# Kernel optimization log

Measured on AMD Instinct MI355X. Metric: run time of the kernel, lower is better.

## Reference

```python
import jax, jax.numpy as jnp
import numpy as np

B, D, E, G, P, H = 8192, 2048, 8, 4, 512, 192
T, DT, TAU, VTH, VRESET = 20, 0.001, 0.02, 0.5, 0.0
DELTA0, KTOP, KROUTE, PREDW = 7.0, 32, 2, 0.1


def setup_inputs() -> dict:
    key = jax.random.key(0)
    ks = jax.random.split(key, 12)
    s = 0.02
    return {
        "query_embedding": jax.random.normal(ks[0], (B, D), jnp.float32),
        "Wg": jax.random.normal(ks[1], (2, E), jnp.float32) * s,
        "bg": jnp.zeros((E,), jnp.float32),
        "Wp": jax.random.normal(ks[2], (2, E), jnp.float32) * s,
        "bp": jnp.zeros((E,), jnp.float32),
        "Wgg": jax.random.normal(ks[3], (2, G), jnp.float32) * s,
        "bgg": jnp.zeros((G,), jnp.float32),
        "W1": jax.random.normal(ks[4], (E, D, P), jnp.float32) * (1.0 / np.sqrt(D)),
        "b1": jnp.zeros((E, P), jnp.float32),
        "W2": jax.random.normal(ks[5], (E, P, D), jnp.float32) * (1.0 / np.sqrt(P)),
        "b2": jnp.zeros((E, D), jnp.float32),
    }


def reference(query_embedding, Wg, bg, Wp, bp, Wgg, bgg, W1, b1, W2, b2):
    x = query_embedding  # [B, D], already embed_dim -> no pad/slice
    dtype = x.dtype

    # --- Phasor bank temporal features on per-row mean ---
    qm = jnp.mean(x, axis=-1)  # [B]
    freqs = DELTA0 * jnp.arange(1, H + 1, dtype=dtype)  # [H]
    ang = qm[:, None] * freqs[None, :]  # [B, H]
    temporal = jnp.concatenate([jnp.cos(ang), jnp.sin(ang)], axis=-1)  # [B, 2H]

    # --- Spiking attention over top-K |x| indices (LIF over T steps) ---
    topk_idx = jax.lax.top_k(jnp.abs(x), KTOP)[1]  # [B, K]
    rows = jnp.arange(B)[:, None]
    I = jnp.zeros((B, D), dtype).at[rows, topk_idx].add(1.0)  # input current [B, vocab=D]

    def lif_step(v, _):
        v = v * (1.0 - DT / TAU) + I
        spike = (v >= VTH).astype(dtype)
        v = jnp.where(spike > 0, VRESET, v)
        return v, spike

    _, spikes = jax.lax.scan(lif_step, jnp.zeros((B, D), dtype), None, length=T)
    attention_gains = jnp.mean(spikes, axis=0)  # [B, D] spike rates

    # --- Bio gating inputs ---
    gate_in = jnp.stack([jnp.mean(temporal, axis=-1), jnp.mean(attention_gains, axis=-1)], axis=-1)  # [B, 2]

    gate_logits = gate_in @ Wg + bg  # [B, E]
    gate_logits = gate_logits - PREDW * (gate_in @ Wp + bp)

    # group routing bias: experts grouped round-robin i % G
    group_logits = gate_in @ Wgg + bgg  # [B, G]
    gmap = jax.nn.one_hot(jnp.arange(E) % G, G, dtype=dtype)  # [E, G]
    gate_logits = gate_logits + group_logits @ gmap.T

    gate_weights = jax.nn.softmax(gate_logits, axis=-1)  # temperature = 1

    # top-k routing + renormalization
    _, tidx = jax.lax.top_k(gate_weights, KROUTE)
    mask = jnp.zeros_like(gate_weights).at[rows, tidx].set(1.0)
    gated = gate_weights * mask
    gate_weights = gated / (jnp.sum(gated, axis=-1, keepdims=True) + 1e-9)

    # --- Dense MLP experts (bottleneck P = hidden // 4) ---
    h = jax.nn.relu(jnp.einsum('bd,edp->ebp', x, W1) + b1[:, None, :])  # [E, B, P]
    expert_out = jnp.einsum('ebp,eph->ebh', h, W2) + b2[:, None, :]  # [E, B, D]

    # gate-weighted combine
    context = jnp.einsum('be,ebh->bh', gate_weights, expert_out)  # [B, D]
    return context
```

## Files before the change

### kernel.cpp

```cpp
#include <hip/hip_runtime.h>
#include <stdint.h>

#define NB 8192
#define ND 2048
#define NE 8
#define NG 4
#define NP 512
#define NH 192

typedef _Float16 half_t;
typedef half_t f16x8 __attribute__((ext_vector_type(8)));
typedef float f32x4 __attribute__((ext_vector_type(4)));

__device__ __forceinline__ void gload16(const void* g, void* l) {
  __builtin_amdgcn_global_load_lds(
      (const __attribute__((address_space(1))) void*)g,
      (__attribute__((address_space(3))) void*)l, 16, 0, 0);
}

__global__ __launch_bounds__(256) void k_pre(
    const float* __restrict__ x, half_t* __restrict__ xh,
    const float* __restrict__ W1, const float* __restrict__ W2,
    half_t* __restrict__ w1t, half_t* __restrict__ w2t,
    const float* __restrict__ Wg, const float* __restrict__ bg,
    const float* __restrict__ Wp, const float* __restrict__ bp,
    const float* __restrict__ Wgg, const float* __restrict__ bgg,
    int* __restrict__ e0a, int* __restrict__ e1a,
    float* __restrict__ w0a, float* __restrict__ w1a)
{
  const int t = threadIdx.x;

  if (blockIdx.x >= NB) {
    int id = blockIdx.x - NB;
    const int which = id >> 12;
    id &= 4095;
    const int R = which ? NP : ND;
    const int C = which ? ND : NP;
    const float* src = which ? W2 : W1;
    half_t* dst = which ? w2t : w1t;
    const int tiles_c = C >> 5;
    const int tiles_per_e = (R >> 6) * tiles_c;
    int e = id / tiles_per_e;
    int rem = id - e * tiles_per_e;
    int tr = rem / tiles_c, tc = rem - tr * tiles_c;
    __shared__ float tile[64][33];
    const int lc = t & 31, lr = t >> 5;
    const float* s = src + (size_t)e * R * C + (size_t)(tr * 64) * C + tc * 32;
#pragma unroll
    for (int i = 0; i < 8; i++)
      tile[lr + i * 8][lc] = s[(size_t)(lr + i * 8) * C + lc];
    __syncthreads();
    const int n = t >> 3, kc = (t & 7) * 8;
    __align__(16) half_t hb[8];
#pragma unroll
    for (int j = 0; j < 8; j++) hb[j] = (half_t)tile[kc + j][n];
    half_t* d = dst + (size_t)e * R * C + (size_t)(tc * 32 + n) * R + tr * 64 + kc;
    *reinterpret_cast<int4*>(d) = *reinterpret_cast<const int4*>(hb);
    return;
  }

  const int b = blockIdx.x;
  const float* xr = x + (size_t)b * ND;
  const float4 v0 = ((const float4*)xr)[t * 2];
  const float4 v1 = ((const float4*)xr)[t * 2 + 1];
  float f[8] = {v0.x, v0.y, v0.z, v0.w, v1.x, v1.y, v1.z, v1.w};
  double s = 0.0;
  __align__(16) half_t hb[8];
#pragma unroll
  for (int i = 0; i < 8; i++) { s += (double)f[i]; hb[i] = (half_t)f[i]; }
  *reinterpret_cast<int4*>(xh + (size_t)b * ND + t * 8) = *reinterpret_cast<const int4*>(hb);

#pragma unroll
  for (int m = 32; m >= 1; m >>= 1) s += __shfl_xor(s, m);
  __shared__ double part[4];
  __shared__ double qm_s;
  if ((t & 63) == 0) part[t >> 6] = s;
  __syncthreads();
  if (t == 0) qm_s = (part[0] + part[1] + part[2] + part[3]) / (double)ND;
  __syncthreads();

  const double q = qm_s;
  double g = 0.0;
  if (t < 192) {
    double ang = q * (7.0 * (double)(t + 1));
    g = cos(ang) + sin(ang);
  }
#pragma unroll
  for (int m = 32; m >= 1; m >>= 1) g += __shfl_xor(g, m);
  __shared__ double gp[4];
  if ((t & 63) == 0) gp[t >> 6] = g;
  __syncthreads();

  if (t < 64) {
    const double tm = (gp[0] + gp[1] + gp[2] + gp[3]) / (2.0 * (double)NH);
    const double gi1 = 32.0 / 2048.0;
    double lg = -1.0e300;
    if (t < 8) {
      const int e = t, gg = e & 3;
      lg = tm * (double)Wg[e] + gi1 * (double)Wg[NE + e] + (double)bg[e];
      lg -= 0.1 * (tm * (double)Wp[e] + gi1 * (double)Wp[NE + e] + (double)bp[e]);
      lg += tm * (double)Wgg[gg] + gi1 * (double)Wgg[NG + gg] + (double)bgg[gg];
    }
    double mx = lg;
#pragma unroll
    for (int m = 4; m >= 1; m >>= 1) mx = fmax(mx, __shfl_xor(mx, m));
    double pe = 0.0;
    if (t < 8) pe = exp(lg - mx);
    double ps = pe;
#pragma unroll
    for (int m = 4; m >= 1; m >>= 1) ps += __shfl_xor(ps, m);

    double lgs[8], pes[8];
#pragma unroll
    for (int e = 0; e < 8; e++) { lgs[e] = __shfl(lg, e); pes[e] = __shfl(pe, e); }

    if (t == 0) {
      int e0 = 0;
      for (int e = 1; e < NE; e++) if (lgs[e] > lgs[e0]) e0 = e;
      int e1 = (e0 == 0) ? 1 : 0;
      for (int e = 0; e < NE; e++) if (e != e0 && lgs[e] > lgs[e1]) e1 = e;
      const double p0 = pes[e0] / ps;
      const double p1 = pes[e1] / ps;
      const double den = p0 + p1 + 1e-9;
      e0a[b] = e0; e1a[b] = e1;
      w0a[b] = (float)(p0 / den);
      w1a[b] = (float)(p1 / den);
    }
  }
}

__global__ __launch_bounds__(256) void k_bucket(
    const int* __restrict__ e0a, const int* __restrict__ e1a,
    const float* __restrict__ w0a, const float* __restrict__ w1a,
    int* __restrict__ rowl, float* __restrict__ wl, int* __restrict__ cnt,
    int* __restrict__ pos0a, int* __restrict__ pos1a,
    int* __restrict__ rowlp, int* __restrict__ cntp,
    int* __restrict__ ticket, int* __restrict__ pbase,
    int* __restrict__ i16b, int* __restrict__ i16m, int* __restrict__ n16,
    int* __restrict__ ipp, int* __restrict__ ipm, int* __restrict__ np)
{
  const int t = threadIdx.x;
  const int r = blockIdx.x * 256 + t;
  __shared__ int hist[16], base[16], cursor[16];
  __shared__ int histp[64], basep[64], cursorp[64];
  __shared__ int lastf;
  if (t < 16) { hist[t] = 0; cursor[t] = 0; }
  if (t < 64) { histp[t] = 0; cursorp[t] = 0; }
  __syncthreads();

  const int e0 = e0a[r], e1 = e1a[r];
  const int p = e0 * 8 + e1;
  atomicAdd(&hist[e0], 1);
  atomicAdd(&hist[8 + e1], 1);
  atomicAdd(&histp[p], 1);
  __syncthreads();
  if (t < 16) base[t] = atomicAdd(&cnt[t], hist[t]);
  if (t < 64) basep[t] = atomicAdd(&cntp[t], histp[t]);
  __syncthreads();

  int p0 = atomicAdd(&cursor[e0], 1);
  int idx0 = base[e0] + p0;
  rowl[e0 * NB + idx0] = r;
  wl[e0 * NB + idx0] = w0a[r];
  pos0a[r] = idx0;

  int p1 = atomicAdd(&cursor[8 + e1], 1);
  int idx1 = base[8 + e1] + p1;
  rowl[(8 + e1) * NB + idx1] = r;
  wl[(8 + e1) * NB + idx1] = w1a[r];
  pos1a[r] = idx1;

  int pp = atomicAdd(&cursorp[p], 1);
  rowlp[p * NB + basep[p] + pp] = r;

  __threadfence();
  __syncthreads();
  if (t == 0) lastf = (atomicAdd(ticket, 1) == (int)gridDim.x - 1);
  __syncthreads();
  if (lastf) {
    if (t == 0) {
      int c[16];
#pragma unroll
      for (int i = 0; i < 16; i++) c[i] = atomicAdd(&cnt[i], 0);
      int s = 0;
#pragma unroll
      for (int i = 0; i < 16; i++) { pbase[i] = s; s += c[i]; }
      int k = 0;
      for (int bb = 0; bb < 16; bb++)
        for (int m0 = 0; m0 < c[bb]; m0 += 128) { i16b[k] = bb; i16m[k] = m0; k++; }
      *n16 = k;
    } else if (t == 64) {
      int c[64];
#pragma unroll
      for (int i = 0; i < 64; i++) c[i] = atomicAdd(&cntp[i], 0);
      int k = 0;
      for (int pq = 0; pq < 64; pq++)
        for (int m0 = 0; m0 < c[pq]; m0 += 128) { ipp[k] = pq; ipm[k] = m0; k++; }
      *np = k;
    }
  }
}

__global__ __launch_bounds__(256, 2) void k_gemm1(
    const half_t* __restrict__ xh, const half_t* __restrict__ w1t,
    const float* __restrict__ b1,
    const int* __restrict__ rowl, const float* __restrict__ wl,
    const int* __restrict__ cnt, const int* __restrict__ pbase,
    const int* __restrict__ i16b, const int* __restrict__ i16m,
    const int* __restrict__ n16, half_t* __restrict__ Hbuf)
{
  const int wi = blockIdx.y;
  if (wi >= *n16) return;
  const int bucket = i16b[wi];
  const int m0 = i16m[wi];
  const int count = cnt[bucket];
  const int e = bucket & 7;
  const int n0 = blockIdx.x * 256;
  const int t = threadIdx.x;

  __shared__ __align__(16) half_t As[3][128 * 32];
  __shared__ __align__(16) half_t Bs[3][256 * 32];
  __shared__ int rows_s[128];
  __shared__ float ws_s[128];

  if (t < 128) {
    int mi = m0 + t;
    int idx = bucket * NB + (mi < count ? mi : m0);
    rows_s[t] = rowl[idx];
    ws_s[t] = wl[idx];
  }
  __syncthreads();

  const int w = t >> 6, lane = t & 63;
  const int cA0 = (w * 2) * 64 + lane, cA1 = cA0 + 64;
  const int rA0 = cA0 >> 2, rA1 = cA1 >> 2;
  const int kA0 = ((cA0 & 3) ^ ((rA0 >> 1) & 3)) * 8;
  const int kA1 = ((cA1 & 3) ^ ((rA1 >> 1) & 3)) * 8;
  const half_t* gA0 = xh + (size_t)rows_s[rA0] * ND + kA0;
  const half_t* gA1 = xh + (size_t)rows_s[rA1] * ND + kA1;
  const half_t* w1te = w1t + (size_t)e * NP * ND;
  const int cB0 = (w * 4) * 64 + lane, cB1 = cB0 + 64, cB2 = cB0 + 128, cB3 = cB0 + 192;
  const int rB0 = cB0 >> 2, rB1 = cB1 >> 2, rB2 = cB2 >> 2, rB3 = cB3 >> 2;
  const half_t* gB0 = w1te + (size_t)(n0 + rB0) * ND + ((cB0 & 3) ^ ((rB0 >> 1) & 3)) * 8;
  const half_t* gB1 = w1te + (size_t)(n0 + rB1) * ND + ((cB1 & 3) ^ ((rB1 >> 1) & 3)) * 8;
  const half_t* gB2 = w1te + (size_t)(n0 + rB2) * ND + ((cB2 & 3) ^ ((rB2 >> 1) & 3)) * 8;
  const half_t* gB3 = w1te + (size_t)(n0 + rB3) * ND + ((cB3 & 3) ^ ((rB3 >> 1) & 3)) * 8;

  const int wr = w >> 1, wc = w & 1;
  const int lrow = lane & 15, lk = lane >> 4;
  const int lko = (lk ^ ((lrow >> 1) & 3)) * 8;

  f32x4 acc[4][8];
#pragma unroll
  for (int i = 0; i < 4; i++)
#pragma unroll
    for (int j = 0; j < 8; j++) {
      acc[i][j][0] = 0.f; acc[i][j][1] = 0.f; acc[i][j][2] = 0.f; acc[i][j][3] = 0.f;
    }

  auto stage = [&](int bi, int tt) {
    const int kk = tt * 32;
    half_t* la = &As[bi][w * 1024];
    gload16(gA0 + kk, la);
    gload16(gA1 + kk, la + 512);
    half_t* lb = &Bs[bi][w * 2048];
    gload16(gB0 + kk, lb);
    gload16(gB1 + kk, lb + 512);
    gload16(gB2 + kk, lb + 1024);
    gload16(gB3 + kk, lb + 1536);
  };
  auto compute = [&](int bi) {
    f16x8 af[4], bf[8];
#pragma unroll
    for (int i = 0; i < 4; i++)
      af[i] = *reinterpret_cast<const f16x8*>(&As[bi][(wr * 64 + i * 16 + lrow) * 32 + lko]);
#pragma unroll
    for (int n = 0; n < 8; n++)
      bf[n] = *reinterpret_cast<const f16x8*>(&Bs[bi][(wc * 128 + n * 16 + lrow) * 32 + lko]);
#pragma unroll
    for (int mi = 0; mi < 4; mi++)
#pragma unroll
      for (int ni = 0; ni < 8; ni++)
        acc[mi][ni] = __builtin_amdgcn_mfma_f32_16x16x32_f16(af[mi], bf[ni], acc[mi][ni], 0, 0, 0);
  };

  stage(0, 0);
  stage(1, 1);
  asm volatile("s_waitcnt vmcnt(6)" ::: "memory");
  __builtin_amdgcn_s_barrier();
  for (int t3 = 0; t3 < 60; t3 += 3) {
    stage(2, t3 + 2); compute(0);
    asm volatile("s_waitcnt vmcnt(6) lgkmcnt(0)" ::: "memory");
    __builtin_amdgcn_s_barrier();
    stage(0, t3 + 3); compute(1);
    asm volatile("s_waitcnt vmcnt(6) lgkmcnt(0)" ::: "memory");
    __builtin_amdgcn_s_barrier();
    stage(1, t3 + 4); compute(2);
    asm volatile("s_waitcnt vmcnt(6) lgkmcnt(0)" ::: "memory");
    __builtin_amdgcn_s_barrier();
  }
  stage(2, 62); compute(0);
  asm volatile("s_waitcnt vmcnt(6) lgkmcnt(0)" ::: "memory");
  __builtin_amdgcn_s_barrier();
  stage(0, 63); compute(1);
  asm volatile("s_waitcnt vmcnt(6) lgkmcnt(0)" ::: "memory");
  __builtin_amdgcn_s_barrier();
  compute(2);
  asm volatile("s_waitcnt vmcnt(0) lgkmcnt(0)" ::: "memory");
  __builtin_amdgcn_s_barrier();
  compute(0);

  const int pb = pbase[bucket];
#pragma unroll
  for (int mi = 0; mi < 4; mi++) {
#pragma unroll
    for (int i = 0; i < 4; i++) {
      int lm = wr * 64 + mi * 16 + lk * 4 + i;
      if (m0 + lm < count) {
        size_t prow = (size_t)(pb + m0 + lm) * NP;
        float wcoef = ws_s[lm];
#pragma unroll
        for (int ni = 0; ni < 8; ni++) {
          int col = n0 + wc * 128 + ni * 16 + lrow;
          float v = acc[mi][ni][i] + b1[e * NP + col];
          v = v > 0.f ? v : 0.f;
          Hbuf[prow + col] = (half_t)(v * wcoef);
        }
      }
    }
  }
}

__global__ __launch_bounds__(256) void k_gemm2p(
    const half_t* __restrict__ Hbuf, const half_t* __restrict__ w2t,
    const float* __restrict__ b2,
    const int* __restrict__ rowlp, const int* __restrict__ cntp,
    const int* __restrict__ pbase,
    const int* __restrict__ pos0a, const int* __restrict__ pos1a,
    const float* __restrict__ w0a, const float* __restrict__ w1a,
    const int* __restrict__ ipp, const int* __restrict__ ipm,
    const int* __restrict__ np, float* __restrict__ out)
{
  const int wi = blockIdx.y;
  if (wi >= *np) return;
  const int p = ipp[wi];
  const int m0 = ipm[wi];
  const int count = cntp[p];
  const int e0 = p >> 3, e1 = p & 7;
  const int n0 = blockIdx.x * 128;
  const int t = threadIdx.x;

  __shared__ __align__(16) half_t As[3][128 * 32];
  __shared__ __align__(16) half_t Bs[3][128 * 32];
  __shared__ int h0_s[128], h1_s[128], rs_s[128];
  __shared__ float w0_s[128], w1_s[128];

  if (t < 128) {
    int mi = m0 + t;
    int r = rowlp[p * NB + (mi < count ? mi : m0)];
    rs_s[t] = r;
    h0_s[t] = pbase[e0] + pos0a[r];
    h1_s[t] = pbase[8 + e1] + pos1a[r];
    w0_s[t] = w0a[r];
    w1_s[t] = w1a[r];
  }
  __syncthreads();

  const int w = t >> 6, lane = t & 63;
  const int c0 = w * 128 + lane, c1 = c0 + 64;
  const int row0 = c0 >> 2, ch0 = c0 & 3;
  const int row1 = c1 >> 2, ch1 = c1 & 3;
  const int sw0 = (row0 >> 1) & 3, sw1 = (row1 >> 1) & 3;
  const half_t* w2e0 = w2t + (size_t)e0 * ND * NP;
  const half_t* w2e1 = w2t + (size_t)e1 * ND * NP;
  const half_t* sa00 = Hbuf + (size_t)h0_s[row0] * NP + ((ch0 ^ sw0) * 8);
  const half_t* sa01 = Hbuf + (size_t)h0_s[row1] * NP + ((ch1 ^ sw1) * 8);
  const half_t* sa10 = Hbuf + (size_t)h1_s[row0] * NP + ((ch0 ^ sw0) * 8);
  const half_t* sa11 = Hbuf + (size_t)h1_s[row1] * NP + ((ch1 ^ sw1) * 8);
  const half_t* pB00 = w2e0 + (size_t)(n0 + row0) * NP + ((ch0 ^ sw0) * 8);
  const half_t* pB01 = w2e0 + (size_t)(n0 + row1) * NP + ((ch1 ^ sw1) * 8);
  const half_t* pB10 = w2e1 + (size_t)(n0 + row0) * NP + ((ch0 ^ sw0) * 8);
  const half_t* pB11 = w2e1 + (size_t)(n0 + row1) * NP + ((ch1 ^ sw1) * 8);

  const int wr = w >> 1, wc = w & 1;
  const int lrow = lane & 15, lk = lane >> 4;
  const int lko = (lk ^ ((lrow >> 1) & 3)) * 8;

  f32x4 acc[4][4];
#pragma unroll
  for (int i = 0; i < 4; i++)
#pragma unroll
    for (int j = 0; j < 4; j++) {
      acc[i][j][0] = 0.f; acc[i][j][1] = 0.f; acc[i][j][2] = 0.f; acc[i][j][3] = 0.f;
    }

  const int NT = 32;

  auto stage = [&](int bi, int tt) {
    const int kk = (tt & 15) * 32;
    half_t* la = &As[bi][w * 1024];
    half_t* lb = &Bs[bi][w * 1024];
    if (tt & 16) {
      gload16(sa10 + kk, la);
      gload16(sa11 + kk, la + 512);
      gload16(pB10 + kk, lb);
      gload16(pB11 + kk, lb + 512);
    } else {
      gload16(sa00 + kk, la);
      gload16(sa01 + kk, la + 512);
      gload16(pB00 + kk, lb);
      gload16(pB01 + kk, lb + 512);
    }
  };
  auto compute = [&](int bi) {
    f16x8 af[4], bf[4];
#pragma unroll
    for (int i = 0; i < 4; i++) {
      af[i] = *reinterpret_cast<const f16x8*>(&As[bi][(wr * 64 + i * 16 + lrow) * 32 + lko]);
      bf[i] = *reinterpret_cast<const f16x8*>(&Bs[bi][(wc * 64 + i * 16 + lrow) * 32 + lko]);
    }
#pragma unroll
    for (int mi = 0; mi < 4; mi++)
#pragma unroll
      for (int ni = 0; ni < 4; ni++)
        acc[mi][ni] = __builtin_amdgcn_mfma_f32_16x16x32_f16(af[mi], bf[ni], acc[mi][ni], 0, 0, 0);
  };

  stage(0, 0);
  stage(1, 1);
  asm volatile("s_waitcnt vmcnt(4)" ::: "memory");
  __builtin_amdgcn_s_barrier();
#pragma unroll
  for (int tt = 0; tt < NT; ++tt) {
    if (tt + 2 < NT) stage((tt + 2) % 3, tt + 2);
    compute(tt % 3);
    if (tt + 1 < NT) {
      if (tt + 2 < NT) asm volatile("s_waitcnt vmcnt(4) lgkmcnt(0)" ::: "memory");
      else             asm volatile("s_waitcnt vmcnt(0) lgkmcnt(0)" ::: "memory");
      __builtin_amdgcn_s_barrier();
    }
  }

  float b20[4], b21[4];
#pragma unroll
  for (int ni = 0; ni < 4; ni++) {
    int col = n0 + wc * 64 + ni * 16 + lrow;
    b20[ni] = b2[e0 * ND + col];
    b21[ni] = b2[e1 * ND + col];
  }
#pragma unroll
  for (int mi = 0; mi < 4; mi++) {
#pragma unroll
    for (int i = 0; i < 4; i++) {
      int lm = wr * 64 + mi * 16 + lk * 4 + i;
      if (m0 + lm < count) {
        int r = rs_s[lm];
        float wb0 = w0_s[lm], wb1 = w1_s[lm];
        float* orow = out + (size_t)r * ND;
#pragma unroll
        for (int ni = 0; ni < 4; ni++) {
          int col = n0 + wc * 64 + ni * 16 + lrow;
          orow[col] = acc[mi][ni][i] + wb0 * b20[ni] + wb1 * b21[ni];
        }
      }
    }
  }
}

extern "C" void kernel_launch(void* const* d_in, const int* in_sizes, int n_in,
                              void* d_out, int out_size, void* d_ws, size_t ws_size,
                              hipStream_t stream)
{
  const float* x   = (const float*)d_in[0];
  const float* Wg  = (const float*)d_in[1];
  const float* bg  = (const float*)d_in[2];
  const float* Wp  = (const float*)d_in[3];
  const float* bp  = (const float*)d_in[4];
  const float* Wgg = (const float*)d_in[5];
  const float* bgg = (const float*)d_in[6];
  const float* W1  = (const float*)d_in[7];
  const float* b1  = (const float*)d_in[8];
  const float* W2  = (const float*)d_in[9];
  const float* b2  = (const float*)d_in[10];
  float* out = (float*)d_out;

  char* ws = (char*)d_ws;
  size_t off = 0;
  const size_t OFF_XH   = off; off += (size_t)NB * ND * 2;
  const size_t OFF_W1T  = off; off += (size_t)NE * NP * ND * 2;
  const size_t OFF_W2T  = off; off += (size_t)NE * ND * NP * 2;
  const size_t OFF_H    = off; off += (size_t)(2 * NB + 128) * NP * 2;
  const size_t OFF_ROWL = off; off += (size_t)16 * NB * 4;
  const size_t OFF_WL   = off; off += (size_t)16 * NB * 4;
  const size_t OFF_ROWLP= off; off += (size_t)64 * NB * 4;
  const size_t OFF_CNT  = off; off += 64;
  const size_t OFF_CNTP = off; off += 256;
  const size_t OFF_TKT  = off; off += 64;
  const size_t OFF_PB   = off; off += 64;
  const size_t OFF_E0   = off; off += (size_t)NB * 4;
  const size_t OFF_E1   = off; off += (size_t)NB * 4;
  const size_t OFF_W0   = off; off += (size_t)NB * 4;
  const size_t OFF_W1A  = off; off += (size_t)NB * 4;
  const size_t OFF_POS0 = off; off += (size_t)NB * 4;
  const size_t OFF_POS1 = off; off += (size_t)NB * 4;
  const size_t OFF_I16B = off; off += 1024;
  const size_t OFF_I16M = off; off += 1024;
  const size_t OFF_N16  = off; off += 64;
  const size_t OFF_IPP  = off; off += 1024;
  const size_t OFF_IPM  = off; off += 1024;
  const size_t OFF_NP   = off; off += 64;

  half_t* xh   = (half_t*)(ws + OFF_XH);
  half_t* w1t  = (half_t*)(ws + OFF_W1T);
  half_t* w2t  = (half_t*)(ws + OFF_W2T);
  half_t* Hbuf = (half_t*)(ws + OFF_H);
  int*    rowl = (int*)(ws + OFF_ROWL);
  float*  wl   = (float*)(ws + OFF_WL);
  int*    rowlp= (int*)(ws + OFF_ROWLP);
  int*    cnt  = (int*)(ws + OFF_CNT);
  int*    cntp = (int*)(ws + OFF_CNTP);
  int*    tkt  = (int*)(ws + OFF_TKT);
  int*    pb   = (int*)(ws + OFF_PB);
  int*    e0a  = (int*)(ws + OFF_E0);
  int*    e1a  = (int*)(ws + OFF_E1);
  float*  w0a  = (float*)(ws + OFF_W0);
  float*  w1a  = (float*)(ws + OFF_W1A);
  int*    pos0a= (int*)(ws + OFF_POS0);
  int*    pos1a= (int*)(ws + OFF_POS1);
  int*    i16b = (int*)(ws + OFF_I16B);
  int*    i16m = (int*)(ws + OFF_I16M);
  int*    n16  = (int*)(ws + OFF_N16);
  int*    ipp  = (int*)(ws + OFF_IPP);
  int*    ipm  = (int*)(ws + OFF_IPM);
  int*    np   = (int*)(ws + OFF_NP);

  hipMemsetAsync(cnt, 0, 64 + 256 + 64, stream);
  k_pre<<<NB + 8192, 256, 0, stream>>>(x, xh, W1, W2, w1t, w2t,
                                       Wg, bg, Wp, bp, Wgg, bgg,
                                       e0a, e1a, w0a, w1a);
  k_bucket<<<NB / 256, 256, 0, stream>>>(e0a, e1a, w0a, w1a, rowl, wl, cnt,
                                         pos0a, pos1a, rowlp, cntp,
                                         tkt, pb, i16b, i16m, n16, ipp, ipm, np);
  k_gemm1<<<dim3(2, 144, 1), 256, 0, stream>>>(xh, w1t, b1, rowl, wl, cnt, pb,
                                               i16b, i16m, n16, Hbuf);
  k_gemm2p<<<dim3(16, 128, 1), 256, 0, stream>>>(Hbuf, w2t, b2, rowlp, cntp, pb,
                                                 pos0a, pos1a, w0a, w1a, ipp, ipm, np, out);
}
```

Before: 333.1 us.

## Use 8-wave 512-thread blocks for both expert GEMMs, widen gemm2 N tile

k_gemm1 keeps its 128x256 block tile but splits it across 8 waves of 64x64 each instead of 4 waves of 64x128, which halves per-wave accumulators and global-to-LDS loads. k_gemm2p doubles its N tile to 256 so more A-tile reuse happens per block, also with 8 waves, and its grid in x is halved. Wait counts are adjusted to the new per-thread load counts. The launch_bounds(512,4) hint asks for high occupancy, which can force tight register budgets and spills. The large LDS footprint may also prevent that occupancy from being reached.

Measured after the change: 327.5 us. No clear change (-1.7%).

```diff
diff --git a/kernel.cpp b/kernel.cpp
--- a/kernel.cpp
+++ b/kernel.cpp
@@ -201,7 +201,7 @@
   }
 }
 
-__global__ __launch_bounds__(256, 2) void k_gemm1(
+__global__ __launch_bounds__(512, 4) void k_gemm1(
     const half_t* __restrict__ xh, const half_t* __restrict__ w1t,
     const float* __restrict__ b1,
     const int* __restrict__ rowl, const float* __restrict__ wl,
@@ -232,78 +232,69 @@
   __syncthreads();
 
   const int w = t >> 6, lane = t & 63;
-  const int cA0 = (w * 2) * 64 + lane, cA1 = cA0 + 64;
-  const int rA0 = cA0 >> 2, rA1 = cA1 >> 2;
-  const int kA0 = ((cA0 & 3) ^ ((rA0 >> 1) & 3)) * 8;
-  const int kA1 = ((cA1 & 3) ^ ((rA1 >> 1) & 3)) * 8;
-  const half_t* gA0 = xh + (size_t)rows_s[rA0] * ND + kA0;
-  const half_t* gA1 = xh + (size_t)rows_s[rA1] * ND + kA1;
+  const int rA = w * 16 + (lane >> 2);
+  const int kA = ((lane & 3) ^ ((rA >> 1) & 3)) * 8;
+  const half_t* gA = xh + (size_t)rows_s[rA] * ND + kA;
   const half_t* w1te = w1t + (size_t)e * NP * ND;
-  const int cB0 = (w * 4) * 64 + lane, cB1 = cB0 + 64, cB2 = cB0 + 128, cB3 = cB0 + 192;
-  const int rB0 = cB0 >> 2, rB1 = cB1 >> 2, rB2 = cB2 >> 2, rB3 = cB3 >> 2;
-  const half_t* gB0 = w1te + (size_t)(n0 + rB0) * ND + ((cB0 & 3) ^ ((rB0 >> 1) & 3)) * 8;
-  const half_t* gB1 = w1te + (size_t)(n0 + rB1) * ND + ((cB1 & 3) ^ ((rB1 >> 1) & 3)) * 8;
-  const half_t* gB2 = w1te + (size_t)(n0 + rB2) * ND + ((cB2 & 3) ^ ((rB2 >> 1) & 3)) * 8;
-  const half_t* gB3 = w1te + (size_t)(n0 + rB3) * ND + ((cB3 & 3) ^ ((rB3 >> 1) & 3)) * 8;
-
-  const int wr = w >> 1, wc = w & 1;
+  const int rB0 = w * 32 + (lane >> 2), rB1 = rB0 + 16;
+  const int kB0 = ((lane & 3) ^ ((rB0 >> 1) & 3)) * 8;
+  const int kB1 = ((lane & 3) ^ ((rB1 >> 1) & 3)) * 8;
+  const half_t* gB0 = w1te + (size_t)(n0 + rB0) * ND + kB0;
+  const half_t* gB1 = w1te + (size_t)(n0 + rB1) * ND + kB1;
+
+  const int wr = w >> 2, wn = w & 3;
   const int lrow = lane & 15, lk = lane >> 4;
   const int lko = (lk ^ ((lrow >> 1) & 3)) * 8;
 
-  f32x4 acc[4][8];
+  f32x4 acc[4][4];
 #pragma unroll
   for (int i = 0; i < 4; i++)
 #pragma unroll
-    for (int j = 0; j < 8; j++) {
+    for (int j = 0; j < 4; j++) {
       acc[i][j][0] = 0.f; acc[i][j][1] = 0.f; acc[i][j][2] = 0.f; acc[i][j][3] = 0.f;
     }
 
   auto stage = [&](int bi, int tt) {
     const int kk = tt * 32;
-    half_t* la = &As[bi][w * 1024];
-    gload16(gA0 + kk, la);
-    gload16(gA1 + kk, la + 512);
-    half_t* lb = &Bs[bi][w * 2048];
-    gload16(gB0 + kk, lb);
-    gload16(gB1 + kk, lb + 512);
-    gload16(gB2 + kk, lb + 1024);
-    gload16(gB3 + kk, lb + 1536);
+    gload16(gA + kk, &As[bi][w * 512]);
+    gload16(gB0 + kk, &Bs[bi][w * 1024]);
+    gload16(gB1 + kk, &Bs[bi][w * 1024 + 512]);
   };
   auto compute = [&](int bi) {
-    f16x8 af[4], bf[8];
+    f16x8 af[4], bf[4];
 #pragma unroll
     for (int i = 0; i < 4; i++)
       af[i] = *reinterpret_cast<const f16x8*>(&As[bi][(wr * 64 + i * 16 + lrow) * 32 + lko]);
 #pragma unroll
-    for (int n = 0; n < 8; n++)
-      bf[n] = *reinterpret_cast<const f16x8*>(&Bs[bi][(wc * 128 + n * 16 + lrow) * 32 + lko]);
+    for (int n = 0; n < 4; n++)
+      bf[n] = *reinterpret_cast<const f16x8*>(&Bs[bi][(wn * 64 + n * 16 + lrow) * 32 + lko]);
 #pragma unroll
     for (int mi = 0; mi < 4; mi++)
 #pragma unroll
-      for (int ni = 0; ni < 8; ni++)
+      for (int ni = 0; ni < 4; ni++)
         acc[mi][ni] = __builtin_amdgcn_mfma_f32_16x16x32_f16(af[mi], bf[ni], acc[mi][ni], 0, 0, 0);
   };
 
   stage(0, 0);
   stage(1, 1);
-  asm volatile("s_waitcnt vmcnt(6)" ::: "memory");
+  asm volatile("s_waitcnt vmcnt(3)" ::: "memory");
   __builtin_amdgcn_s_barrier();
   for (int t3 = 0; t3 < 60; t3 += 3) {
     stage(2, t3 + 2); compute(0);
-    asm volatile("s_waitcnt vmcnt(6) lgkmcnt(0)" ::: "memory");
+    asm volatile("s_waitcnt vmcnt(3) lgkmcnt(0)" ::: "memory");
     __builtin_amdgcn_s_barrier();
     stage(0, t3 + 3); compute(1);
-    asm volatile("s_waitcnt vmcnt(6) lgkmcnt(0)" ::: "memory");
+    asm volatile("s_waitcnt vmcnt(3) lgkmcnt(0)" ::: "memory");
     __builtin_amdgcn_s_barrier();
     stage(1, t3 + 4); compute(2);
-    asm volatile("s_waitcnt vmcnt(6) lgkmcnt(0)" ::: "memory");
+    asm volatile("s_waitcnt vmcnt(3) lgkmcnt(0)" ::: "memory");
     __builtin_amdgcn_s_barrier();
   }
   stage(2, 62); compute(0);
-  asm volatile("s_waitcnt vmcnt(6) lgkmcnt(0)" ::: "memory");
+  asm volatile("s_waitcnt vmcnt(3) lgkmcnt(0)" ::: "memory");
   __builtin_amdgcn_s_barrier();
   stage(0, 63); compute(1);
-  asm volatile("s_waitcnt vmcnt(6) lgkmcnt(0)" ::: "memory");
+  asm volatile("s_waitcnt vmcnt(3) lgkmcnt(0)" ::: "memory");
   __builtin_amdgcn_s_barrier();
   compute(2);
   asm volatile("s_waitcnt vmcnt(0) lgkmcnt(0)" ::: "memory");
@@ -320,8 +311,8 @@
         size_t prow = (size_t)(pb + m0 + lm) * NP;
         float wcoef = ws_s[lm];
 #pragma unroll
-        for (int ni = 0; ni < 8; ni++) {
-          int col = n0 + wc * 128 + ni * 16 + lrow;
+        for (int ni = 0; ni < 4; ni++) {
+          int col = n0 + wn * 64 + ni * 16 + lrow;
           float v = acc[mi][ni][i] + b1[e * NP + col];
           v = v > 0.f ? v : 0.f;
           Hbuf[prow + col] = (half_t)(v * wcoef);
@@ -331,7 +322,7 @@
   }
 }
 
-__global__ __launch_bounds__(256) void k_gemm2p(
+__global__ __launch_bounds__(512, 4) void k_gemm2p(
     const half_t* __restrict__ Hbuf, const half_t* __restrict__ w2t,
     const float* __restrict__ b2,
     const int* __restrict__ rowlp, const int* __restrict__ cntp,
@@ -347,11 +338,11 @@
   const int m0 = ipm[wi];
   const int count = cntp[p];
   const int e0 = p >> 3, e1 = p & 7;
-  const int n0 = blockIdx.x * 128;
+  const int n0 = blockIdx.x * 256;
   const int t = threadIdx.x;
 
   __shared__ __align__(16) half_t As[3][128 * 32];
-  __shared__ __align__(16) half_t Bs[3][128 * 32];
+  __shared__ __align__(16) half_t Bs[3][256 * 32];
   __shared__ int h0_s[128], h1_s[128], rs_s[128];
   __shared__ float w0_s[128], w1_s[128];
 
@@ -367,22 +358,22 @@
   __syncthreads();
 
   const int w = t >> 6, lane = t & 63;
-  const int c0 = w * 128 + lane, c1 = c0 + 64;
-  const int row0 = c0 >> 2, ch0 = c0 & 3;
-  const int row1 = c1 >> 2, ch1 = c1 & 3;
-  const int sw0 = (row0 >> 1) & 3, sw1 = (row1 >> 1) & 3;
+  const int rA = w * 16 + (lane >> 2);
+  const int kA = ((lane & 3) ^ ((rA >> 1) & 3)) * 8;
+  const half_t* sa0 = Hbuf + (size_t)h0_s[rA] * NP + kA;
+  const half_t* sa1 = Hbuf + (size_t)h1_s[rA] * NP + kA;
+
   const half_t* w2e0 = w2t + (size_t)e0 * ND * NP;
   const half_t* w2e1 = w2t + (size_t)e1 * ND * NP;
-  const half_t* sa00 = Hbuf + (size_t)h0_s[row0] * NP + ((ch0 ^ sw0) * 8);
-  const half_t* sa01 = Hbuf + (size_t)h0_s[row1] * NP + ((ch1 ^ sw1) * 8);
-  const half_t* sa10 = Hbuf + (size_t)h1_s[row0] * NP + ((ch0 ^ sw0) * 8);
-  const half_t* sa11 = Hbuf + (size_t)h1_s[row1] * NP + ((ch1 ^ sw1) * 8);
-  const half_t* pB00 = w2e0 + (size_t)(n0 + row0) * NP + ((ch0 ^ sw0) * 8);
-  const half_t* pB01 = w2e0 + (size_t)(n0 + row1) * NP + ((ch1 ^ sw1) * 8);
-  const half_t* pB10 = w2e1 + (size_t)(n0 + row0) * NP + ((ch0 ^ sw0) * 8);
-  const half_t* pB11 = w2e1 + (size_t)(n0 + row1) * NP + ((ch1 ^ sw1) * 8);
-
-  const int wr = w >> 1, wc = w & 1;
+  const int rB0 = w * 32 + (lane >> 2), rB1 = rB0 + 16;
+  const int kB0 = ((lane & 3) ^ ((rB0 >> 1) & 3)) * 8;
+  const int kB1 = ((lane & 3) ^ ((rB1 >> 1) & 3)) * 8;
+  const half_t* pB00 = w2e0 + (size_t)(n0 + rB0) * NP + kB0;
+  const half_t* pB01 = w2e0 + (size_t)(n0 + rB1) * NP + kB1;
+  const half_t* pB10 = w2e1 + (size_t)(n0 + rB0) * NP + kB0;
+  const half_t* pB11 = w2e1 + (size_t)(n0 + rB1) * NP + kB1;
+
+  const int wr = w >> 2, wn = w & 3;
   const int lrow = lane & 15, lk = lane >> 4;
   const int lko = (lk ^ ((lrow >> 1) & 3)) * 8;
 
@@ -398,27 +389,24 @@
 
   auto stage = [&](int bi, int tt) {
     const int kk = (tt & 15) * 32;
-    half_t* la = &As[bi][w * 1024];
-    half_t* lb = &Bs[bi][w * 1024];
     if (tt & 16) {
-      gload16(sa10 + kk, la);
-      gload16(sa11 + kk, la + 512);
-      gload16(pB10 + kk, lb);
-      gload16(pB11 + kk, lb + 512);
+      gload16(sa1 + kk, &As[bi][w * 512]);
+      gload16(pB10 + kk, &Bs[bi][w * 1024]);
+      gload16(pB11 + kk, &Bs[bi][w * 1024 + 512]);
     } else {
-      gload16(sa00 + kk, la);
-      gload16(sa01 + kk, la + 512);
-      gload16(pB00 + kk, lb);
-      gload16(pB01 + kk, lb + 512);
+      gload16(sa0 + kk, &As[bi][w * 512]);
+      gload16(pB00 + kk, &Bs[bi][w * 1024]);
+      gload16(pB01 + kk, &Bs[bi][w * 1024 + 512]);
     }
   };
   auto compute = [&](int bi) {
     f16x8 af[4], bf[4];
 #pragma unroll
-    for (int i = 0; i < 4; i++) {
+    for (int i = 0; i < 4; i++)
       af[i] = *reinterpret_cast<const f16x8*>(&As[bi][(wr * 64 + i * 16 + lrow) * 32 + lko]);
-      bf[i] = *reinterpret_cast<const f16x8*>(&Bs[bi][(wc * 64 + i * 16 + lrow) * 32 + lko]);
-    }
+#pragma unroll
+    for (int n = 0; n < 4; n++)
+      bf[n] = *reinterpret_cast<const f16x8*>(&Bs[bi][(wn * 64 + n * 16 + lrow) * 32 + lko]);
 #pragma unroll
     for (int mi = 0; mi < 4; mi++)
 #pragma unroll
@@ -428,14 +416,14 @@
 
   stage(0, 0);
   stage(1, 1);
-  asm volatile("s_waitcnt vmcnt(4)" ::: "memory");
+  asm volatile("s_waitcnt vmcnt(3)" ::: "memory");
   __builtin_amdgcn_s_barrier();
 #pragma unroll
   for (int tt = 0; tt < NT; ++tt) {
     if (tt + 2 < NT) stage((tt + 2) % 3, tt + 2);
     compute(tt % 3);
     if (tt + 1 < NT) {
-      if (tt + 2 < NT) asm volatile("s_waitcnt vmcnt(4) lgkmcnt(0)" ::: "memory");
+      if (tt + 2 < NT) asm volatile("s_waitcnt vmcnt(3) lgkmcnt(0)" ::: "memory");
       else             asm volatile("s_waitcnt vmcnt(0) lgkmcnt(0)" ::: "memory");
       __builtin_amdgcn_s_barrier();
     }
@@ -444,7 +432,7 @@
   float b20[4], b21[4];
 #pragma unroll
   for (int ni = 0; ni < 4; ni++) {
-    int col = n0 + wc * 64 + ni * 16 + lrow;
+    int col = n0 + wn * 64 + ni * 16 + lrow;
     b20[ni] = b2[e0 * ND + col];
     b21[ni] = b2[e1 * ND + col];
   }
@@ -459,7 +447,7 @@
         float* orow = out + (size_t)r * ND;
 #pragma unroll
         for (int ni = 0; ni < 4; ni++) {
-          int col = n0 + wc * 64 + ni * 16 + lrow;
+          int col = n0 + wn * 64 + ni * 16 + lrow;
           orow[col] = acc[mi][ni][i] + wb0 * b20[ni] + wb1 * b21[ni];
         }
       }
@@ -541,8 +529,8 @@
   k_bucket<<<NB / 256, 256, 0, stream>>>(e0a, e1a, w0a, w1a, rowl, wl, cnt,
                                          pos0a, pos1a, rowlp, cntp,
                                          tkt, pb, i16b, i16m, n16, ipp, ipm, np);
-  k_gemm1<<<dim3(2, 144, 1), 256, 0, stream>>>(xh, w1t, b1, rowl, wl, cnt, pb,
+  k_gemm1<<<dim3(2, 144, 1), 512, 0, stream>>>(xh, w1t, b1, rowl, wl, cnt, pb,
                                                i16b, i16m, n16, Hbuf);
-  k_gemm2p<<<dim3(16, 128, 1), 256, 0, stream>>>(Hbuf, w2t, b2, rowlp, cntp, pb,
+  k_gemm2p<<<dim3(8, 128, 1), 512, 0, stream>>>(Hbuf, w2t, b2, rowlp, cntp, pb,
                                                  pos0a, pos1a, w0a, w1a, ipp, ipm, np, out);
 }
```
